# Optimization experiments

Hardware: AMD Instinct MI355X
Metric: run time of the kernel (lower is better)

The kernel has to match this reference:

```python
import jax, jax.numpy as jnp
import numpy as np

HEADS = 8
DIM_HEAD = 64
SCALE = DIM_HEAD ** -0.5
QUERY_DIM = 512
CTX_DIM = 64
INNER = HEADS * DIM_HEAD  # 512
GATE_HID = 32


def setup_inputs() -> dict:
    key = jax.random.key(0)
    ks = jax.random.split(key, 11)
    B, N, M = 4, 2048, 2048
    s = lambda fan: 1.0 / np.sqrt(fan)
    return {
        "x": jax.random.normal(ks[0], (B, N, QUERY_DIM), dtype=jnp.float32),
        "context": jax.random.normal(ks[1], (B, M, CTX_DIM), dtype=jnp.float32),
        "Wq": jax.random.normal(ks[2], (QUERY_DIM, INNER), dtype=jnp.float32) * s(QUERY_DIM),
        "Wk": jax.random.normal(ks[3], (CTX_DIM, INNER), dtype=jnp.float32) * s(CTX_DIM),
        "Wv": jax.random.normal(ks[4], (CTX_DIM, INNER), dtype=jnp.float32) * s(CTX_DIM),
        "W1": jax.random.normal(ks[5], (CTX_DIM, GATE_HID), dtype=jnp.float32) * s(CTX_DIM),
        "b1": jnp.zeros((GATE_HID,), dtype=jnp.float32),
        "W2": jax.random.normal(ks[6], (GATE_HID, 1), dtype=jnp.float32) * s(GATE_HID),
        "b2": jnp.zeros((1,), dtype=jnp.float32),
        "Wo": jax.random.normal(ks[7], (INNER, QUERY_DIM), dtype=jnp.float32) * s(INNER),
        "bo": jnp.zeros((QUERY_DIM,), dtype=jnp.float32),
    }


def reference(x, context, Wq, Wk, Wv, W1, b1, W2, b2, Wo, bo):
    B, N, _ = x.shape
    M = context.shape[1]
    # visual reliability gate: sigmoid(relu(ctx @ W1 + b1) @ W2 + b2) -> [B, M, 1]
    gate = jax.nn.sigmoid(jax.nn.relu(context @ W1 + b1) @ W2 + b2)
    ctx = context * gate
    # projections
    q = (x @ Wq).reshape(B, N, HEADS, DIM_HEAD).transpose(0, 2, 1, 3)    # [B,H,N,D]
    k = (ctx @ Wk).reshape(B, M, HEADS, DIM_HEAD).transpose(0, 2, 1, 3)  # [B,H,M,D]
    v = (ctx @ Wv).reshape(B, M, HEADS, DIM_HEAD).transpose(0, 2, 1, 3)  # [B,H,M,D]
    # scaled dot-product attention (full score matrix, as in source)
    sim = jnp.einsum('bhid,bhjd->bhij', q, k) * SCALE
    attn = jax.nn.softmax(sim, axis=-1)
    out = jnp.einsum('bhij,bhjd->bhid', attn, v)
    out = out.transpose(0, 2, 1, 3).reshape(B, N, INNER)
    return out @ Wo + bo
```

## Files before the change

### kernel.cpp

```cpp
#include <hip/hip_runtime.h>

typedef unsigned short u16;
typedef unsigned int u32;
using frag16 = __attribute__((ext_vector_type(8))) short;
using facc   = __attribute__((ext_vector_type(4))) float;
using facc16 = __attribute__((ext_vector_type(16))) float;

#define DEV static __device__ __forceinline__

DEV u16 f2bf(float f) {
  union { float f; unsigned u; } v; v.f = f;
  unsigned r = v.u + 0x7fffu + ((v.u >> 16) & 1u);
  return (u16)(r >> 16);
}
DEV unsigned fbits(float f) {
  union { float f; unsigned u; } v; v.f = f;
  return v.u;
}
DEV unsigned pkbf(float lo, float hi) {
  return __builtin_amdgcn_perm(fbits(hi) + 0x8000u, fbits(lo) + 0x8000u, 0x07060302u);
}
DEV void gld16(const u16* g, u16* l) {
  __builtin_amdgcn_global_load_lds(
      (__attribute__((address_space(1))) unsigned int*)(g),
      (__attribute__((address_space(3))) unsigned int*)(l), 16, 0, 0);
}

__global__ __launch_bounds__(256) void prep_gate_kernel(const float4* __restrict__ x,
    const float* __restrict__ Wq, const float* __restrict__ Wk,
    const float* __restrict__ Wv, const float* __restrict__ Wo,
    const float* __restrict__ ctx, const float* __restrict__ W1,
    const float* __restrict__ b1, const float* __restrict__ W2,
    const float* __restrict__ b2,
    u16* __restrict__ xb, u16* __restrict__ WqT, u16* __restrict__ WkT,
    u16* __restrict__ WvT, u16* __restrict__ WoT, u16* __restrict__ gctx) {
  int bid = blockIdx.x;
  if (bid < 4096) {
    int id = bid * 256 + threadIdx.x;
    float4 v = x[id];
    ushort4 o;
    o.x = f2bf(v.x); o.y = f2bf(v.y); o.z = f2bf(v.z); o.w = f2bf(v.w);
    *(ushort4*)(xb + (size_t)id * 4) = o;
  } else if (bid < 6400) {
    int id = (bid - 4096) * 256 + threadIdx.x;
    const float* W; u16* WT; int K, idx;
    if (id < 262144)      { W = Wq; WT = WqT; K = 512; idx = id; }
    else if (id < 294912) { W = Wk; WT = WkT; K = 64;  idx = id - 262144; }
    else if (id < 327680) { W = Wv; WT = WvT; K = 64;  idx = id - 294912; }
    else                  { W = Wo; WT = WoT; K = 512; idx = id - 327680; }
    int n = idx / K, k = idx - n * K;
    WT[idx] = f2bf(W[k * 512 + n]);
  } else {
    int wave = threadIdx.x >> 6, lane = threadIdx.x & 63;
    int row = (bid - 6400) * 4 + wave;
    __shared__ float sc[4][64];
    float cv = ctx[(size_t)row * 64 + lane];
    sc[wave][lane] = cv;
    __syncthreads();
    float h = 0.f;
    if (lane < 32) {
      h = b1[lane];
      #pragma unroll
      for (int i = 0; i < 64; ++i) h += sc[wave][i] * W1[i * 32 + lane];
      h = fmaxf(h, 0.f) * W2[lane];
    }
    #pragma unroll
    for (int off = 32; off; off >>= 1) h += __shfl_xor(h, off);
    float g = 1.f / (1.f + __expf(-(h + b2[0])));
    gctx[(size_t)row * 64 + lane] = f2bf(cv * g);
  }
}

template<int MODE>
DEV void gemm128_body(const u16* __restrict__ A, const u16* __restrict__ BT,
                      void* __restrict__ Cp, const float* __restrict__ bias,
                      int m0, int n0, float scale,
                      u16* As0, u16* As1, u16* Bs0, u16* Bs1) {
  const int K = 512, N = 512;
  const int lane = threadIdx.x & 63, wave = threadIdx.x >> 6;
  const int quad = lane >> 4, l16 = lane & 15;
  const int wr = wave >> 1, wc = wave & 1;

  const u16* gA = A + (size_t)(m0 + wave * 32 + (lane >> 2)) * K + (lane & 3) * 8;
  const u16* gB = BT + (size_t)(n0 + wave * 16 + (lane >> 2)) * K + (lane & 3) * 8;

  facc acc[4][2] = {};

  for (int k0 = 0; k0 < K; k0 += 64) {
    if (k0) __syncthreads();
    gld16(gA + k0,           As0 + wave * 1024);
    gld16(gA + 16 * K + k0,  As0 + wave * 1024 + 512);
    gld16(gA + k0 + 32,          As1 + wave * 1024);
    gld16(gA + 16 * K + k0 + 32, As1 + wave * 1024 + 512);
    gld16(gB + k0,      Bs0 + wave * 512);
    gld16(gB + k0 + 32, Bs1 + wave * 512);
    __syncthreads();

    #pragma unroll
    for (int hh = 0; hh < 2; ++hh) {
      const u16* Ah = hh ? As1 : As0;
      const u16* Bh = hh ? Bs1 : Bs0;
      frag16 af[4], bf[2];
      #pragma unroll
      for (int rt = 0; rt < 4; ++rt)
        af[rt] = *(const frag16*)(Ah + (wr * 64 + rt * 16 + l16) * 32 + quad * 8);
      #pragma unroll
      for (int ct = 0; ct < 2; ++ct)
        bf[ct] = *(const frag16*)(Bh + (wc * 32 + ct * 16 + l16) * 32 + quad * 8);
      #pragma unroll
      for (int rt = 0; rt < 4; ++rt)
        #pragma unroll
        for (int ct = 0; ct < 2; ++ct)
          acc[rt][ct] = __builtin_amdgcn_mfma_f32_16x16x32_bf16(af[rt], bf[ct], acc[rt][ct], 0, 0, 0);
    }
  }

  #pragma unroll
  for (int rt = 0; rt < 4; ++rt) {
    #pragma unroll
    for (int ct = 0; ct < 2; ++ct) {
      int col = n0 + wc * 32 + ct * 16 + l16;
      int r0g = m0 + wr * 64 + rt * 16 + quad * 4;
      if (MODE == 0) {
        u16* C = (u16*)Cp;
        #pragma unroll
        for (int r = 0; r < 4; ++r)
          C[(size_t)(r0g + r) * N + col] = f2bf(acc[rt][ct][r] * scale);
      } else {
        float* C = (float*)Cp;
        float bv = bias[col];
        #pragma unroll
        for (int r = 0; r < 4; ++r)
          C[(size_t)(r0g + r) * N + col] = acc[rt][ct][r] + bv;
      }
    }
  }
}

__global__ __launch_bounds__(256) void proj_kernel(const u16* __restrict__ xb,
    const u16* __restrict__ WqT, u16* __restrict__ qb,
    const u16* __restrict__ gctx, const u16* __restrict__ BkT,
    const u16* __restrict__ BvT, u16* __restrict__ Kp, u16* __restrict__ Vp) {
  __shared__ __align__(16) u16 As0[128 * 32], As1[128 * 32];
  __shared__ __align__(16) u16 Bs0[64 * 32], Bs1[64 * 32];
  int bid = blockIdx.x;
  if (bid < 512) {
    int n0 = (bid & 7) * 64, m0 = (bid >> 3) * 128;
    gemm128_body<0>(xb, WqT, qb, nullptr, m0, n0,
                    0.125f * 1.4426950408889634f, As0, As1, Bs0, Bs1);
    return;
  }
  bid -= 512;
  const int Kd = 64;
  int lane = threadIdx.x & 63, wave = threadIdx.x >> 6;
  int quad = lane >> 4, l16 = lane & 15;
  int wr = wave >> 1, wc = wave & 1;
  int rowBase = (bid >> 3) * 64 + wr * 32;
  int colBase = (bid & 7) * 64 + wc * 32;
  facc ak[2][2] = {}, av[2][2] = {};
  const u16* a0 = gctx + (size_t)(rowBase + l16) * Kd + quad * 8;
  const u16* a1 = a0 + (size_t)16 * Kd;
  const u16* bk0 = BkT + (size_t)(colBase + l16) * Kd + quad * 8;
  const u16* bk1 = bk0 + (size_t)16 * Kd;
  const u16* bv0 = BvT + (size_t)(colBase + l16) * Kd + quad * 8;
  const u16* bv1 = bv0 + (size_t)16 * Kd;
  #pragma unroll
  for (int kk = 0; kk < Kd; kk += 32) {
    frag16 af0 = *(const frag16*)(a0 + kk);
    frag16 af1 = *(const frag16*)(a1 + kk);
    frag16 k0 = *(const frag16*)(bk0 + kk);
    frag16 k1 = *(const frag16*)(bk1 + kk);
    frag16 v0 = *(const frag16*)(bv0 + kk);
    frag16 v1 = *(const frag16*)(bv1 + kk);
    ak[0][0] = __builtin_amdgcn_mfma_f32_16x16x32_bf16(af0, k0, ak[0][0], 0, 0, 0);
    ak[0][1] = __builtin_amdgcn_mfma_f32_16x16x32_bf16(af0, k1, ak[0][1], 0, 0, 0);
    ak[1][0] = __builtin_amdgcn_mfma_f32_16x16x32_bf16(af1, k0, ak[1][0], 0, 0, 0);
    ak[1][1] = __builtin_amdgcn_mfma_f32_16x16x32_bf16(af1, k1, ak[1][1], 0, 0, 0);
    av[0][0] = __builtin_amdgcn_mfma_f32_16x16x32_bf16(af0, v0, av[0][0], 0, 0, 0);
    av[0][1] = __builtin_amdgcn_mfma_f32_16x16x32_bf16(af0, v1, av[0][1], 0, 0, 0);
    av[1][0] = __builtin_amdgcn_mfma_f32_16x16x32_bf16(af1, v0, av[1][0], 0, 0, 0);
    av[1][1] = __builtin_amdgcn_mfma_f32_16x16x32_bf16(af1, v1, av[1][1], 0, 0, 0);
  }
  #pragma unroll
  for (int rt = 0; rt < 2; ++rt) {
    #pragma unroll
    for (int ct = 0; ct < 2; ++ct) {
      int col = colBase + ct * 16 + l16;
      int r0g = rowBase + rt * 16 + quad * 4;
      int hh = col >> 6, d = col & 63;
      int b = r0g >> 11;
      #pragma unroll
      for (int r = 0; r < 4; ++r) {
        int m = (r0g + r) & 2047;
        size_t addr = ((((size_t)(b * 8 + hh) * 64 + (m >> 5)) * 4 + (d >> 4)) * 64
                       + ((d >> 3) & 1) * 32 + (m & 31)) * 8 + (d & 7);
        Kp[addr] = f2bf(ak[rt][ct][r]);
      }
      int m = r0g & 2047;
      size_t addr = ((((size_t)(b * 8 + hh) * 64 + (m >> 5)) * 4
                      + ((m >> 4) & 1) * 2 + (d >> 5)) * 64
                     + ((m >> 3) & 1) * 32 + (d & 31)) * 8 + (m & 7);
      ushort4 o;
      o.x = f2bf(av[rt][ct][0]); o.y = f2bf(av[rt][ct][1]);
      o.z = f2bf(av[rt][ct][2]); o.w = f2bf(av[rt][ct][3]);
      *(ushort4*)(Vp + addr) = o;
    }
  }
}

__global__ __launch_bounds__(256, 2) void attn_kernel(
    const u16* __restrict__ qb, const u16* __restrict__ Kp,
    const u16* __restrict__ Vp, u16* __restrict__ ob) {
  const int lane = threadIdx.x & 63, wave = threadIdx.x >> 6;
  const int l32 = lane & 31;
  const int hi = lane >> 5;
  const int bid = blockIdx.x;
  const int bh = bid & 31;
  const int qblk = bid >> 5;
  const int b = bh >> 3, h = bh & 7;
  const int q0 = (qblk * 4 + wave) * 32;
  const int rowg = b * 2048 + q0 + l32;

  __shared__ __align__(16) u16 sK[2][2][2048], sV[2][2][2048];

  const u16* qp = qb + (size_t)rowg * 512 + h * 64 + hi * 8;
  frag16 qf0 = *(const frag16*)(qp);
  frag16 qf1 = *(const frag16*)(qp + 16);
  frag16 qf2 = *(const frag16*)(qp + 32);
  frag16 qf3 = *(const frag16*)(qp + 48);

  facc16 O0 = {}, O1 = {};
  float lsum = 0.f;

  const size_t ts = 2048;
  const u16* kpb = Kp + (size_t)(bh * 64) * ts + wave * 512 + lane * 8;
  const u16* vpb = Vp + (size_t)(bh * 64) * ts + wave * 512 + lane * 8;

  gld16(kpb,      sK[0][0] + wave * 512);
  gld16(kpb + ts, sK[0][1] + wave * 512);
  gld16(vpb,      sV[0][0] + wave * 512);
  gld16(vpb + ts, sV[0][1] + wave * 512);

  for (int g = 0; g < 32; ++g) {
    const int p = g & 1;
    __syncthreads();
    if (g + 1 < 32) {
      const size_t t2 = (size_t)(2 * g + 2) * ts;
      gld16(kpb + t2,      sK[p ^ 1][0] + wave * 512);
      gld16(kpb + t2 + ts, sK[p ^ 1][1] + wave * 512);
      gld16(vpb + t2,      sV[p ^ 1][0] + wave * 512);
      gld16(vpb + t2 + ts, sV[p ^ 1][1] + wave * 512);
    }

    frag16 kfa[4], kfb[4];
    #pragma unroll
    for (int i = 0; i < 4; ++i) {
      kfa[i] = *(const frag16*)(sK[p][0] + i * 512 + lane * 8);
      kfb[i] = *(const frag16*)(sK[p][1] + i * 512 + lane * 8);
    }

    facc16 Sa = {}, Sb = {};
    Sa = __builtin_amdgcn_mfma_f32_32x32x16_bf16(kfa[0], qf0, Sa, 0, 0, 0);
    Sb = __builtin_amdgcn_mfma_f32_32x32x16_bf16(kfb[0], qf0, Sb, 0, 0, 0);
    Sa = __builtin_amdgcn_mfma_f32_32x32x16_bf16(kfa[1], qf1, Sa, 0, 0, 0);
    Sb = __builtin_amdgcn_mfma_f32_32x32x16_bf16(kfb[1], qf1, Sb, 0, 0, 0);
    Sa = __builtin_amdgcn_mfma_f32_32x32x16_bf16(kfa[2], qf2, Sa, 0, 0, 0);
    Sb = __builtin_amdgcn_mfma_f32_32x32x16_bf16(kfb[2], qf2, Sb, 0, 0, 0);
    Sa = __builtin_amdgcn_mfma_f32_32x32x16_bf16(kfa[3], qf3, Sa, 0, 0, 0);
    Sb = __builtin_amdgcn_mfma_f32_32x32x16_bf16(kfb[3], qf3, Sb, 0, 0, 0);

    float ea[16], eb[16];
    #pragma unroll
    for (int r = 0; r < 16; ++r) { ea[r] = __builtin_amdgcn_exp2f(Sa[r]);
                                   eb[r] = __builtin_amdgcn_exp2f(Sb[r]); }
    #pragma unroll
    for (int r = 0; r < 16; ++r) lsum += ea[r] + eb[r];

    unsigned pua[2][4], pub[2][4];
    #pragma unroll
    for (int c = 0; c < 2; ++c) {
      {
        const float* ee = ea + c * 8;
        unsigned L0 = pkbf(ee[0], ee[1]);
        unsigned L1 = pkbf(ee[2], ee[3]);
        unsigned H0 = pkbf(ee[4], ee[5]);
        unsigned H1 = pkbf(ee[6], ee[7]);
        unsigned Y0 = hi ? L0 : H0;
        unsigned Y1 = hi ? L1 : H1;
        unsigned X0 = (unsigned)__shfl_xor((int)Y0, 32);
        unsigned X1 = (unsigned)__shfl_xor((int)Y1, 32);
        pua[c][0] = hi ? X0 : L0;
        pua[c][1] = hi ? X1 : L1;
        pua[c][2] = hi ? H0 : X0;
        pua[c][3] = hi ? H1 : X1;
      }
      {
        const float* ee = eb + c * 8;
        unsigned L0 = pkbf(ee[0], ee[1]);
        unsigned L1 = pkbf(ee[2], ee[3]);
        unsigned H0 = pkbf(ee[4], ee[5]);
        unsigned H1 = pkbf(ee[6], ee[7]);
        unsigned Y0 = hi ? L0 : H0;
        unsigned Y1 = hi ? L1 : H1;
        unsigned X0 = (unsigned)__shfl_xor((int)Y0, 32);
        unsigned X1 = (unsigned)__shfl_xor((int)Y1, 32);
        pub[c][0] = hi ? X0 : L0;
        pub[c][1] = hi ? X1 : L1;
        pub[c][2] = hi ? H0 : X0;
        pub[c][3] = hi ? H1 : X1;
      }
    }
    frag16 Pa0 = *(frag16*)&pua[0][0];
    frag16 Pa1 = *(frag16*)&pua[1][0];
    frag16 Pb0 = *(frag16*)&pub[0][0];
    frag16 Pb1 = *(frag16*)&pub[1][0];

    frag16 vfa[4], vfb[4];
    #pragma unroll
    for (int i = 0; i < 4; ++i) {
      vfa[i] = *(const frag16*)(sV[p][0] + i * 512 + lane * 8);
      vfb[i] = *(const frag16*)(sV[p][1] + i * 512 + lane * 8);
    }

    O0 = __builtin_amdgcn_mfma_f32_32x32x16_bf16(vfa[0], Pa0, O0, 0, 0, 0);
    O1 = __builtin_amdgcn_mfma_f32_32x32x16_bf16(vfa[1], Pa0, O1, 0, 0, 0);
    O0 = __builtin_amdgcn_mfma_f32_32x32x16_bf16(vfa[2], Pa1, O0, 0, 0, 0);
    O1 = __builtin_amdgcn_mfma_f32_32x32x16_bf16(vfa[3], Pa1, O1, 0, 0, 0);
    O0 = __builtin_amdgcn_mfma_f32_32x32x16_bf16(vfb[0], Pb0, O0, 0, 0, 0);
    O1 = __builtin_amdgcn_mfma_f32_32x32x16_bf16(vfb[1], Pb0, O1, 0, 0, 0);
    O0 = __builtin_amdgcn_mfma_f32_32x32x16_bf16(vfb[2], Pb1, O0, 0, 0, 0);
    O1 = __builtin_amdgcn_mfma_f32_32x32x16_bf16(vfb[3], Pb1, O1, 0, 0, 0);
  }

  lsum += __shfl_xor(lsum, 32);
  float rinv = 1.0f / lsum;

  u16* op = ob + (size_t)rowg * 512 + h * 64;
  #pragma unroll
  for (int dt = 0; dt < 2; ++dt) {
    #pragma unroll
    for (int rq = 0; rq < 4; ++rq) {
      float v0, v1, v2, v3;
      if (dt == 0) { v0 = O0[rq*4]; v1 = O0[rq*4+1]; v2 = O0[rq*4+2]; v3 = O0[rq*4+3]; }
      else         { v0 = O1[rq*4]; v1 = O1[rq*4+1]; v2 = O1[rq*4+2]; v3 = O1[rq*4+3]; }
      uint2 pk;
      pk.x = pkbf(v0 * rinv, v1 * rinv);
      pk.y = pkbf(v2 * rinv, v3 * rinv);
      int d0 = dt * 32 + 8 * rq + 4 * hi;
      *(uint2*)(op + d0) = pk;
    }
  }
}

__global__ __launch_bounds__(256) void gemm_out(const u16* __restrict__ A,
    const u16* __restrict__ BT, float* __restrict__ C,
    const float* __restrict__ bias) {
  __shared__ __align__(16) u16 As0[128 * 32], As1[128 * 32];
  __shared__ __align__(16) u16 Bs0[64 * 32], Bs1[64 * 32];
  int n0 = (blockIdx.x & 7) * 64, m0 = (blockIdx.x >> 3) * 128;
  gemm128_body<2>(A, BT, C, bias, m0, n0, 1.f, As0, As1, Bs0, Bs1);
}

extern "C" void kernel_launch(void* const* d_in, const int* in_sizes, int n_in,
                              void* d_out, int out_size, void* d_ws, size_t ws_size,
                              hipStream_t stream) {
  const float* x   = (const float*)d_in[0];
  const float* ctx = (const float*)d_in[1];
  const float* Wq  = (const float*)d_in[2];
  const float* Wk  = (const float*)d_in[3];
  const float* Wv  = (const float*)d_in[4];
  const float* W1  = (const float*)d_in[5];
  const float* b1  = (const float*)d_in[6];
  const float* W2  = (const float*)d_in[7];
  const float* b2  = (const float*)d_in[8];
  const float* Wo  = (const float*)d_in[9];
  const float* bo  = (const float*)d_in[10];
  float* out = (float*)d_out;

  char* ws = (char*)d_ws;
  size_t off = 0;
  auto alloc = [&](size_t bytes) {
    char* p = ws + off;
    off += (bytes + 255) & ~(size_t)255;
    return p;
  };
  u16* xb    = (u16*)alloc(8192ull * 512 * 2);
  u16* qb    = (u16*)alloc(8192ull * 512 * 2);
  u16* Kp    = (u16*)alloc(8192ull * 512 * 2);
  u16* Vp    = (u16*)alloc(8192ull * 512 * 2);
  u16* ob    = (u16*)alloc(8192ull * 512 * 2);
  u16* gctx  = (u16*)alloc(8192ull * 64 * 2);
  u16* WqT   = (u16*)alloc(512ull * 512 * 2);
  u16* WkT   = (u16*)alloc(512ull * 64 * 2);
  u16* WvT   = (u16*)alloc(512ull * 64 * 2);
  u16* WoT   = (u16*)alloc(512ull * 512 * 2);

  prep_gate_kernel<<<8448, 256, 0, stream>>>((const float4*)x, Wq, Wk, Wv, Wo,
                                             ctx, W1, b1, W2, b2,
                                             xb, WqT, WkT, WvT, WoT, gctx);
  proj_kernel<<<1536, 256, 0, stream>>>(xb, WqT, qb, gctx, WkT, WvT, Kp, Vp);
  attn_kernel<<<512, 256, 0, stream>>>(qb, Kp, Vp, ob);
  gemm_out<<<512, 256, 0, stream>>>(ob, WoT, out, bo);
}
```

Measured before the change: 172.2 us.

## Tile weight transposes via LDS and compute softmax row sums with MFMA

```diff
diff --git a/kernel.cpp b/kernel.cpp
--- a/kernel.cpp
+++ b/kernel.cpp
@@ -19,6 +19,9 @@
 }
 DEV unsigned pkbf(float lo, float hi) {
   return __builtin_amdgcn_perm(fbits(hi) + 0x8000u, fbits(lo) + 0x8000u, 0x07060302u);
+}
+DEV unsigned pkbf_t(float lo, float hi) {
+  return __builtin_amdgcn_perm(fbits(hi), fbits(lo), 0x07060302u);
 }
 DEV void gld16(const u16* g, u16* l) {
   __builtin_amdgcn_global_load_lds(
@@ -41,18 +44,31 @@
     ushort4 o;
     o.x = f2bf(v.x); o.y = f2bf(v.y); o.z = f2bf(v.z); o.w = f2bf(v.w);
     *(ushort4*)(xb + (size_t)id * 4) = o;
-  } else if (bid < 6400) {
-    int id = (bid - 4096) * 256 + threadIdx.x;
-    const float* W; u16* WT; int K, idx;
-    if (id < 262144)      { W = Wq; WT = WqT; K = 512; idx = id; }
-    else if (id < 294912) { W = Wk; WT = WkT; K = 64;  idx = id - 262144; }
-    else if (id < 327680) { W = Wv; WT = WvT; K = 64;  idx = id - 294912; }
-    else                  { W = Wo; WT = WoT; K = 512; idx = id - 327680; }
-    int n = idx / K, k = idx - n * K;
-    WT[idx] = f2bf(W[k * 512 + n]);
+  } else if (bid < 4240) {
+    int job = bid - 4096;
+    const float* W; u16* WT; int K, tile;
+    if (job < 64)      { W = Wq; WT = WqT; K = 512; tile = job; }
+    else if (job < 72) { W = Wk; WT = WkT; K = 64;  tile = job - 64; }
+    else if (job < 80) { W = Wv; WT = WvT; K = 64;  tile = job - 72; }
+    else               { W = Wo; WT = WoT; K = 512; tile = job - 80; }
+    int tilesK = K >> 6;
+    int tr = tile % tilesK, tc = tile / tilesK;
+    __shared__ float tl[64][65];
+    int c = threadIdx.x & 63, r4 = threadIdx.x >> 6;
+    #pragma unroll
+    for (int it = 0; it < 16; ++it) {
+      int kk = it * 4 + r4;
+      tl[kk][c] = W[(size_t)(tr * 64 + kk) * 512 + tc * 64 + c];
+    }
+    __syncthreads();
+    #pragma unroll
+    for (int it = 0; it < 16; ++it) {
+      int nn = it * 4 + r4;
+      WT[(size_t)(tc * 64 + nn) * K + tr * 64 + c] = f2bf(tl[c][nn]);
+    }
   } else {
     int wave = threadIdx.x >> 6, lane = threadIdx.x & 63;
-    int row = (bid - 6400) * 4 + wave;
+    int row = (bid - 4240) * 4 + wave;
     __shared__ float sc[4][64];
     float cv = ctx[(size_t)row * 64 + lane];
     sc[wave][lane] = cv;
@@ -229,8 +245,11 @@
   frag16 qf2 = *(const frag16*)(qp + 32);
   frag16 qf3 = *(const frag16*)(qp + 48);
 
-  facc16 O0 = {}, O1 = {};
-  float lsum = 0.f;
+  frag16 ones;
+  #pragma unroll
+  for (int i = 0; i < 8; ++i) ones[i] = (short)0x3F80;
+
+  facc16 O0 = {}, O1 = {}, Lacc = {};
 
   const size_t ts = 2048;
   const u16* kpb = Kp + (size_t)(bh * 64) * ts + wave * 512 + lane * 8;
@@ -273,18 +292,16 @@
     #pragma unroll
     for (int r = 0; r < 16; ++r) { ea[r] = __builtin_amdgcn_exp2f(Sa[r]);
                                    eb[r] = __builtin_amdgcn_exp2f(Sb[r]); }
-    #pragma unroll
-    for (int r = 0; r < 16; ++r) lsum += ea[r] + eb[r];
 
     unsigned pua[2][4], pub[2][4];
     #pragma unroll
     for (int c = 0; c < 2; ++c) {
       {
         const float* ee = ea + c * 8;
-        unsigned L0 = pkbf(ee[0], ee[1]);
-        unsigned L1 = pkbf(ee[2], ee[3]);
-        unsigned H0 = pkbf(ee[4], ee[5]);
-        unsigned H1 = pkbf(ee[6], ee[7]);
+        unsigned L0 = pkbf_t(ee[0], ee[1]);
+        unsigned L1 = pkbf_t(ee[2], ee[3]);
+        unsigned H0 = pkbf_t(ee[4], ee[5]);
+        unsigned H1 = pkbf_t(ee[6], ee[7]);
         unsigned Y0 = hi ? L0 : H0;
         unsigned Y1 = hi ? L1 : H1;
         unsigned X0 = (unsigned)__shfl_xor((int)Y0, 32);
@@ -296,10 +313,10 @@
       }
       {
         const float* ee = eb + c * 8;
-        unsigned L0 = pkbf(ee[0], ee[1]);
-        unsigned L1 = pkbf(ee[2], ee[3]);
-        unsigned H0 = pkbf(ee[4], ee[5]);
-        unsigned H1 = pkbf(ee[6], ee[7]);
+        unsigned L0 = pkbf_t(ee[0], ee[1]);
+        unsigned L1 = pkbf_t(ee[2], ee[3]);
+        unsigned H0 = pkbf_t(ee[4], ee[5]);
+        unsigned H1 = pkbf_t(ee[6], ee[7]);
         unsigned Y0 = hi ? L0 : H0;
         unsigned Y1 = hi ? L1 : H1;
         unsigned X0 = (unsigned)__shfl_xor((int)Y0, 32);
@@ -315,6 +332,11 @@
     frag16 Pb0 = *(frag16*)&pub[0][0];
     frag16 Pb1 = *(frag16*)&pub[1][0];
 
+    Lacc = __builtin_amdgcn_mfma_f32_32x32x16_bf16(ones, Pa0, Lacc, 0, 0, 0);
+    Lacc = __builtin_amdgcn_mfma_f32_32x32x16_bf16(ones, Pa1, Lacc, 0, 0, 0);
+    Lacc = __builtin_amdgcn_mfma_f32_32x32x16_bf16(ones, Pb0, Lacc, 0, 0, 0);
+    Lacc = __builtin_amdgcn_mfma_f32_32x32x16_bf16(ones, Pb1, Lacc, 0, 0, 0);
+
     frag16 vfa[4], vfb[4];
     #pragma unroll
     for (int i = 0; i < 4; ++i) {
@@ -332,8 +354,7 @@
     O1 = __builtin_amdgcn_mfma_f32_32x32x16_bf16(vfb[3], Pb1, O1, 0, 0, 0);
   }
 
-  lsum += __shfl_xor(lsum, 32);
-  float rinv = 1.0f / lsum;
+  float rinv = 1.0f / Lacc[0];
 
   u16* op = ob + (size_t)rowg * 512 + h * 64;
   #pragma unroll
@@ -395,7 +416,7 @@
   u16* WvT   = (u16*)alloc(512ull * 64 * 2);
   u16* WoT   = (u16*)alloc(512ull * 512 * 2);
 
-  prep_gate_kernel<<<8448, 256, 0, stream>>>((const float4*)x, Wq, Wk, Wv, Wo,
+  prep_gate_kernel<<<6288, 256, 0, stream>>>((const float4*)x, Wq, Wk, Wv, Wo,
                                              ctx, W1, b1, W2, b2,
                                              xb, WqT, WkT, WvT, WoT, gctx);
   proj_kernel<<<1536, 256, 0, stream>>>(xb, WqT, qb, gctx, WkT, WvT, Kp, Vp);
```

Result: faster. 167.0 us (-3.0%).
